# Kernel optimization log

Hardware: AMD Instinct MI355X
Metric: run time of the kernel (lower is better)

The kernel has to match this reference:

```python
import jax, jax.numpy as jnp
import numpy as np

N_NODES = 50000


def setup_inputs() -> dict:
    key = jax.random.key(0)
    k1, k2, k3, k4 = jax.random.split(key, 4)
    x = jax.random.normal(k1, (N_NODES, 256), dtype=jnp.float32)
    edge_index = jax.random.randint(k2, (2, 800000), 0, N_NODES, dtype=jnp.int64)
    W1 = jax.random.normal(k3, (256, 128), dtype=jnp.float32) * (1.0 / np.sqrt(256))
    b1 = jnp.zeros((128,), dtype=jnp.float32)
    W2 = jax.random.normal(k4, (128, 16), dtype=jnp.float32) * (1.0 / np.sqrt(128))
    b2 = jnp.zeros((16,), dtype=jnp.float32)
    return {"x": x, "edge_index": edge_index, "W1": W1, "b1": b1, "W2": W2, "b2": b2}


def _gcn_norm(edge_index, num_nodes):
    # add self-loops, then symmetric normalization D^-1/2 A D^-1/2 (PyG GCNConv default)
    loop = jnp.arange(num_nodes, dtype=edge_index.dtype)
    src = jnp.concatenate([edge_index[0], loop])
    dst = jnp.concatenate([edge_index[1], loop])
    deg = jax.ops.segment_sum(jnp.ones_like(dst, dtype=jnp.float32), dst, num_segments=num_nodes)
    dinv = jnp.where(deg > 0, jax.lax.rsqrt(deg), 0.0)
    norm = dinv[src] * dinv[dst]  # [E+N]
    return src, dst, norm


def _gcn_conv(h, W, b, src, dst, norm, num_nodes):
    h = h @ W                             # linear before propagate
    msg = h[src] * norm[:, None]          # gather + edge scaling
    agg = jax.ops.segment_sum(msg, dst, num_segments=num_nodes)  # scatter-add
    return agg + b


def reference(x, edge_index, W1, b1, W2, b2):
    n = x.shape[0]
    src, dst, norm = _gcn_norm(edge_index, n)
    h = jax.nn.relu(_gcn_conv(x, W1, b1, src, dst, norm, n))
    # F.dropout(training=False) is identity in eval mode
    out = _gcn_conv(h, W2, b2, src, dst, norm, n)
    return jax.nn.log_softmax(out, axis=1)
```

## Files before the change

### kernel.cpp

```cpp
#include <hip/hip_runtime.h>
#include <hip/hip_bf16.h>
#include <math.h>


#define FIN 256
#define FH  128
#define FO  16
#define ECH_LOG 13
#define ECH (1 << ECH_LOG)
#define NCHUNK 98
#define WPH 6272

typedef unsigned int uint;
typedef unsigned short ushort;
typedef __attribute__((ext_vector_type(8))) short bf16x8;
typedef __attribute__((ext_vector_type(4))) float f32x4;

static __device__ __forceinline__ ushort f2bf(float f) {
    __hip_bfloat16 b = __float2bfloat16(f);
    return *reinterpret_cast<ushort*>(&b);
}
static __device__ __forceinline__ float bf2f(ushort u) {
    return __uint_as_float(((uint)u) << 16);
}

__global__ __launch_bounds__(256) void GCN_wprep_k(const float* __restrict__ W1,
                                                   ushort* __restrict__ whT,
                                                   ushort* __restrict__ wlT) {
    int i = blockIdx.x * 256 + threadIdx.x;
    int k = i >> 7, c = i & 127;
    float w = W1[i];
    ushort hh = f2bf(w);
    ushort hl = f2bf(w - bf2f(hh));
    whT[c * 256 + k] = hh;
    wlT[c * 256 + k] = hl;
}

#define G1_BR 64
#define G1_KC 32

__global__ __launch_bounds__(256, 4) void GCN_histgemm_k(
        const float* __restrict__ x, const ushort* __restrict__ whT,
        const ushort* __restrict__ wlT, ushort* __restrict__ h1,
        const int* __restrict__ edge, uint* __restrict__ cw,
        int* __restrict__ rank,
        int N, int E, int nHist, int nWords, int wph) {
    __shared__ __align__(16) char smem[WPH * 4];
    int tid = threadIdx.x;

    if ((int)blockIdx.x < nHist) {
        int bid = blockIdx.x;
        int half = bid & 1;
        int c = bid >> 1;
        uint* lh = (uint*)smem;
        int w0 = half * wph;
        int wlim = nWords - w0; if (wlim > wph) wlim = wph;
        for (int j = tid; j < wlim; j += 256) lh[j] = 0;
        __syncthreads();
        int base = c << ECH_LOG;
        int lim = base + ECH; if (lim > E) lim = E;
        for (int i = base + tid; i < lim; i += 256) {
            int d = edge[E + i];
            int wd = (d >> 2) - w0;
            if ((unsigned)wd < (unsigned)wlim) {
                int sh = (d & 3) << 3;
                uint old = atomicAdd(&lh[wd], 1u << sh);
                rank[i] = (int)((old >> sh) & 0xFFu);
            }
        }
        __syncthreads();
        for (int j = tid; j < wlim; j += 256)
            cw[(size_t)c * nWords + w0 + j] = lh[j];
        return;
    }

    ushort* xh_s = (ushort*)smem;
    ushort* wh_s = (ushort*)(smem + 4096);
    ushort* wl_s = (ushort*)(smem + 12288);
    int row0 = (blockIdx.x - nHist) * G1_BR;
    int ln = tid & 63;
    int w  = tid >> 6;
    int ln15 = ln & 15;
    int q16  = ln >> 4;

    f32x4 acc[4][2];
    #pragma unroll
    for (int mr = 0; mr < 4; mr++)
        #pragma unroll
        for (int nc = 0; nc < 2; nc++) acc[mr][nc] = (f32x4){0.f, 0.f, 0.f, 0.f};

    for (int kc = 0; kc < FIN; kc += G1_KC) {
        #pragma unroll
        for (int j = 0; j < 2; j++) {
            int u = tid + j * 256;
            int r = u >> 3, kq = u & 7;
            int gr = row0 + r;
            float4 v = make_float4(0.f, 0.f, 0.f, 0.f);
            if (gr < N) v = *(const float4*)&x[(size_t)gr * FIN + kc + kq * 4];
            uint2 hw;
            hw.x = (uint)f2bf(v.x) | ((uint)f2bf(v.y) << 16);
            hw.y = (uint)f2bf(v.z) | ((uint)f2bf(v.w) << 16);
            int byte = (r * 64 + kq * 8) ^ (((r >> 1) & 3) << 4);
            *(uint2*)((char*)xh_s + byte) = hw;
        }
        #pragma unroll
        for (int j = 0; j < 2; j++) {
            int u = tid + j * 256;
            int c = u >> 2, ku = u & 3;
            uint4 vh = *(const uint4*)&whT[(size_t)c * 256 + kc + ku * 8];
            uint4 vl = *(const uint4*)&wlT[(size_t)c * 256 + kc + ku * 8];
            int byte = (c * 64 + ku * 16) ^ (((c >> 1) & 3) << 4);
            *(uint4*)((char*)wh_s + byte) = vh;
            *(uint4*)((char*)wl_s + byte) = vl;
        }
        __syncthreads();

        bf16x8 ah[4], bh[2], bl[2];
        #pragma unroll
        for (int mr = 0; mr < 4; mr++) {
            int r = mr * 16 + ln15;
            int byte = r * 64 + ((q16 * 16) ^ (((r >> 1) & 3) << 4));
            ah[mr] = *(const bf16x8*)((const char*)xh_s + byte);
        }
        #pragma unroll
        for (int nc = 0; nc < 2; nc++) {
            int c = w * 32 + nc * 16 + ln15;
            int byte = c * 64 + ((q16 * 16) ^ (((c >> 1) & 3) << 4));
            bh[nc] = *(const bf16x8*)((const char*)wh_s + byte);
            bl[nc] = *(const bf16x8*)((const char*)wl_s + byte);
        }
        #pragma unroll
        for (int mr = 0; mr < 4; mr++)
            #pragma unroll
            for (int nc = 0; nc < 2; nc++) {
                acc[mr][nc] = __builtin_amdgcn_mfma_f32_16x16x32_bf16(
                    ah[mr], bh[nc], acc[mr][nc], 0, 0, 0);
                acc[mr][nc] = __builtin_amdgcn_mfma_f32_16x16x32_bf16(
                    ah[mr], bl[nc], acc[mr][nc], 0, 0, 0);
            }
        __syncthreads();
    }

    #pragma unroll
    for (int mr = 0; mr < 4; mr++) {
        #pragma unroll
        for (int nc = 0; nc < 2; nc++) {
            int cw2 = w * 32 + nc * 16 + ln15;
            #pragma unroll
            for (int j = 0; j < 4; j++) {
                int gr = row0 + mr * 16 + q16 * 4 + j;
                if (gr < N) h1[(size_t)gr * FH + cw2] = f2bf(acc[mr][nc][j]);
            }
        }
    }
}

__global__ __launch_bounds__(256) void GCN_chpfx_k(uint* __restrict__ cw,
                                                   int* __restrict__ count,
                                                   int* __restrict__ bsum,
                                                   int N, int nWords) {
    __shared__ int part[4][64][4];
    __shared__ int red[64];
    int tid = threadIdx.x;
    int wl = tid & 63, g = tid >> 6;
    int w = blockIdx.x * 64 + wl;
    int c0 = g * 25;
    int c1 = c0 + 25; if (c1 > NCHUNK) c1 = NCHUNK;

    int s0 = 0, s1 = 0, s2 = 0, s3 = 0;
    if (w < nWords) {
        for (int c = c0; c < c1; c++) {
            uint v = cw[(size_t)c * nWords + w];
            s0 += (int)(v & 0xFFu);
            s1 += (int)((v >> 8) & 0xFFu);
            s2 += (int)((v >> 16) & 0xFFu);
            s3 += (int)((v >> 24) & 0xFFu);
        }
    }
    part[g][wl][0] = s0; part[g][wl][1] = s1;
    part[g][wl][2] = s2; part[g][wl][3] = s3;
    __syncthreads();

    int b0 = 0, b1 = 0, b2 = 0, b3 = 0;
    for (int gg = 0; gg < g; gg++) {
        b0 += part[gg][wl][0]; b1 += part[gg][wl][1];
        b2 += part[gg][wl][2]; b3 += part[gg][wl][3];
    }
    if (w < nWords) {
        uint r0 = (uint)b0, r1 = (uint)b1, r2 = (uint)b2, r3 = (uint)b3;
        for (int c = c0; c < c1; c++) {
            uint* p = &cw[(size_t)c * nWords + w];
            uint v = *p;
            *p = (r0 & 0xFFu) | ((r1 & 0xFFu) << 8) | ((r2 & 0xFFu) << 16) | ((r3 & 0xFFu) << 24);
            r0 += v & 0xFFu;
            r1 += (v >> 8) & 0xFFu;
            r2 += (v >> 16) & 0xFFu;
            r3 += (v >> 24) & 0xFFu;
        }
    }
    int local = 0;
    if (g == 3 && w < nWords) {
        int t0 = b0 + s0, t1 = b1 + s1, t2 = b2 + s2, t3 = b3 + s3;
        int d0 = 4 * w;
        if (d0 + 0 < N) count[d0 + 0] = t0;
        if (d0 + 1 < N) count[d0 + 1] = t1;
        if (d0 + 2 < N) count[d0 + 2] = t2;
        if (d0 + 3 < N) count[d0 + 3] = t3;
        local = t0 + t1 + t2 + t3 + 4;
    }
    if (g == 3) red[wl] = local;
    __syncthreads();
    if (tid < 32) { red[tid] += red[tid + 32]; }
    __syncthreads();
    if (tid < 16) { red[tid] += red[tid + 16]; }
    __syncthreads();
    if (tid < 8) { red[tid] += red[tid + 8]; }
    __syncthreads();
    if (tid < 4) { red[tid] += red[tid + 4]; }
    __syncthreads();
    if (tid == 0) bsum[blockIdx.x] = red[0] + red[1] + red[2] + red[3];
}

__global__ __launch_bounds__(256) void GCN_scan2_k(const int* __restrict__ count,
                                                   const int* __restrict__ bsum,
                                                   int2* __restrict__ rd2,
                                                   int2* __restrict__ edata, int N) {
    int tid = threadIdx.x;
    int b = blockIdx.x;
    int d = b * 256 + tid;
    int cnt1 = (d < N) ? count[d] + 1 : 0;

    __shared__ int red[256];
    int offp = 0;
    for (int t = tid; t < b; t += 256) offp += bsum[t];
    red[tid] = offp;
    __syncthreads();
    for (int st = 128; st > 0; st >>= 1) {
        if (tid < st) red[tid] += red[tid + st];
        __syncthreads();
    }
    int blockOff = red[0];
    __syncthreads();

    __shared__ int ssum[256];
    ssum[tid] = cnt1;
    __syncthreads();
    for (int off = 1; off < 256; off <<= 1) {
        int t = (tid >= off) ? ssum[tid - off] : 0;
        __syncthreads();
        ssum[tid] += t;
        __syncthreads();
    }
    int r = blockOff + ssum[tid] - cnt1;

    if (d < N) {
        float dv = rsqrtf((float)cnt1);
        rd2[d] = make_int2(r, __float_as_int(dv));
        edata[r] = make_int2(d, __float_as_int(dv * dv));
    }
    if (b == gridDim.x - 1 && tid == 255) rd2[N] = make_int2(blockOff + ssum[255], 0);
}

__global__ __launch_bounds__(256) void GCN_fill_k(const int* __restrict__ edge,
                                                  const int* __restrict__ rank,
                                                  const uint* __restrict__ cw,
                                                  const int2* __restrict__ rd2,
                                                  int2* __restrict__ edata,
                                                  int E, int nWords) {
    int i = blockIdx.x * 256 + threadIdx.x;
    if (i >= E) return;
    int s = edge[i];
    int d = edge[E + i];
    int rk = rank[i];
    int c = i >> ECH_LOG;
    uint pw = cw[(size_t)c * nWords + (d >> 2)];
    int pfx = (int)((pw >> ((d & 3) << 3)) & 0xFFu);
    int2 rdd = rd2[d];
    float ds = __int_as_float(rd2[s].y);
    edata[rdd.x + 1 + pfx + rk] =
        make_int2(s, __float_as_int(ds * __int_as_float(rdd.y)));
}

__global__ __launch_bounds__(256) void GCN_agg1gemm2_k(
        const ushort* __restrict__ h1, const int2* __restrict__ rd2,
        const int2* __restrict__ ed, const float* __restrict__ b1,
        const float* __restrict__ W2, ushort* __restrict__ h2b, int N) {
    __shared__ float w2s[FH][FO];
    __shared__ float hs[16][FH + 4];
    int tid = threadIdx.x;
    #pragma unroll
    for (int j = 0; j < (FH * FO) / 256; j++) {
        int i = tid + j * 256;
        w2s[i >> 4][i & 15] = W2[i];
    }

    int node0 = blockIdx.x * 16;
    int local = tid >> 4;
    int j = tid & 15;
    int node = node0 + local;

    if (node < N) {
        int beg = rd2[node].x, end = rd2[node + 1].x;
        const uint4* hp = (const uint4*)h1;

        float a[8];
        #pragma unroll
        for (int t = 0; t < 8; t++) a[t] = 0.f;

        int i = beg;
        for (; i + 8 <= end; i += 8) {
            int2 e[8];
            uint4 gg[8];
            #pragma unroll
            for (int t = 0; t < 8; t++) e[t] = ed[i + t];
            #pragma unroll
            for (int t = 0; t < 8; t++) gg[t] = hp[(size_t)e[t].x * 16 + j];
            #pragma unroll
            for (int t = 0; t < 8; t++) {
                float w = __int_as_float(e[t].y);
                #pragma unroll
                for (int q = 0; q < 4; q++) {
                    uint u = (&gg[t].x)[q];
                    a[q*2+0] += __uint_as_float(u << 16) * w;
                    a[q*2+1] += __uint_as_float(u & 0xFFFF0000u) * w;
                }
            }
        }
        for (; i + 4 <= end; i += 4) {
            int2 e0 = ed[i + 0], e1 = ed[i + 1], e2 = ed[i + 2], e3 = ed[i + 3];
            float w0 = __int_as_float(e0.y), w1 = __int_as_float(e1.y);
            float w2 = __int_as_float(e2.y), w3 = __int_as_float(e3.y);
            uint4 g0 = hp[(size_t)e0.x * 16 + j];
            uint4 g1 = hp[(size_t)e1.x * 16 + j];
            uint4 g2 = hp[(size_t)e2.x * 16 + j];
            uint4 g3 = hp[(size_t)e3.x * 16 + j];
            #pragma unroll
            for (int q = 0; q < 4; q++) {
                uint u0 = (&g0.x)[q], u1 = (&g1.x)[q], u2 = (&g2.x)[q], u3 = (&g3.x)[q];
                a[q*2+0] += __uint_as_float(u0 << 16) * w0;
                a[q*2+1] += __uint_as_float(u0 & 0xFFFF0000u) * w0;
                a[q*2+0] += __uint_as_float(u1 << 16) * w1;
                a[q*2+1] += __uint_as_float(u1 & 0xFFFF0000u) * w1;
                a[q*2+0] += __uint_as_float(u2 << 16) * w2;
                a[q*2+1] += __uint_as_float(u2 & 0xFFFF0000u) * w2;
                a[q*2+0] += __uint_as_float(u3 << 16) * w3;
                a[q*2+1] += __uint_as_float(u3 & 0xFFFF0000u) * w3;
            }
        }
        for (; i < end; i++) {
            int2 e = ed[i];
            float w = __int_as_float(e.y);
            uint4 g = hp[(size_t)e.x * 16 + j];
            #pragma unroll
            for (int q = 0; q < 4; q++) {
                uint u = (&g.x)[q];
                a[q*2+0] += __uint_as_float(u << 16) * w;
                a[q*2+1] += __uint_as_float(u & 0xFFFF0000u) * w;
            }
        }

        const float4* bp = (const float4*)b1;
        float4 bb0 = bp[j * 2 + 0];
        float4 bb1 = bp[j * 2 + 1];
        float4 o0, o1;
        o0.x = fmaxf(a[0] + bb0.x, 0.f);
        o0.y = fmaxf(a[1] + bb0.y, 0.f);
        o0.z = fmaxf(a[2] + bb0.z, 0.f);
        o0.w = fmaxf(a[3] + bb0.w, 0.f);
        o1.x = fmaxf(a[4] + bb1.x, 0.f);
        o1.y = fmaxf(a[5] + bb1.y, 0.f);
        o1.z = fmaxf(a[6] + bb1.z, 0.f);
        o1.w = fmaxf(a[7] + bb1.w, 0.f);
        *(float4*)&hs[local][j * 8 + 0] = o0;
        *(float4*)&hs[local][j * 8 + 4] = o1;
    }
    __syncthreads();

    float acc = 0.f;
    #pragma unroll 8
    for (int k = 0; k < FH; k++) acc += hs[local][k] * w2s[k][j];
    if (node < N) h2b[(size_t)node * FO + j] = f2bf(acc);
}

__global__ __launch_bounds__(256) void GCN_agg2_k(const ushort* __restrict__ h2b,
                                                  const int2* __restrict__ rd2,
                                                  const int2* __restrict__ ed,
                                                  const float* __restrict__ b2,
                                                  float* __restrict__ out, int N) {
    int tid = threadIdx.x;
    int node = blockIdx.x * 32 + (tid >> 3);
    if (node >= N) return;
    int f2 = tid & 7;
    int beg = rd2[node].x, end = rd2[node + 1].x;
    const uint* hp = (const uint*)h2b;
    float a0 = 0.f, a1 = 0.f;
    int i = beg;
    for (; i + 8 <= end; i += 8) {
        int2 e[8];
        uint u[8];
        #pragma unroll
        for (int t = 0; t < 8; t++) e[t] = ed[i + t];
        #pragma unroll
        for (int t = 0; t < 8; t++) u[t] = hp[(size_t)e[t].x * 8 + f2];
        #pragma unroll
        for (int t = 0; t < 8; t++) {
            float w = __int_as_float(e[t].y);
            a0 += __uint_as_float(u[t] << 16) * w;
            a1 += __uint_as_float(u[t] & 0xFFFF0000u) * w;
        }
    }
    for (; i + 4 <= end; i += 4) {
        int2 e0 = ed[i + 0], e1 = ed[i + 1], e2 = ed[i + 2], e3 = ed[i + 3];
        uint u0 = hp[(size_t)e0.x * 8 + f2];
        uint u1 = hp[(size_t)e1.x * 8 + f2];
        uint u2 = hp[(size_t)e2.x * 8 + f2];
        uint u3 = hp[(size_t)e3.x * 8 + f2];
        float w0 = __int_as_float(e0.y), w1 = __int_as_float(e1.y);
        float w2 = __int_as_float(e2.y), w3 = __int_as_float(e3.y);
        a0 += __uint_as_float(u0 << 16) * w0 + __uint_as_float(u1 << 16) * w1
            + __uint_as_float(u2 << 16) * w2 + __uint_as_float(u3 << 16) * w3;
        a1 += __uint_as_float(u0 & 0xFFFF0000u) * w0 + __uint_as_float(u1 & 0xFFFF0000u) * w1
            + __uint_as_float(u2 & 0xFFFF0000u) * w2 + __uint_as_float(u3 & 0xFFFF0000u) * w3;
    }
    for (; i < end; i++) {
        int2 e = ed[i];
        uint u = hp[(size_t)e.x * 8 + f2];
        float w = __int_as_float(e.y);
        a0 += __uint_as_float(u << 16) * w;
        a1 += __uint_as_float(u & 0xFFFF0000u) * w;
    }
    float2 bb = ((const float2*)b2)[f2];
    float v0 = a0 + bb.x;
    float v1 = a1 + bb.y;
    float mx = fmaxf(v0, v1);
    #pragma unroll
    for (int m = 4; m >= 1; m >>= 1) mx = fmaxf(mx, __shfl_xor(mx, m, 8));
    float s = expf(v0 - mx) + expf(v1 - mx);
    #pragma unroll
    for (int m = 4; m >= 1; m >>= 1) s += __shfl_xor(s, m, 8);
    float ls = logf(s);
    float2 o = make_float2(v0 - mx - ls, v1 - mx - ls);
    ((float2*)out)[(size_t)node * 8 + f2] = o;
}

extern "C" void kernel_launch(void* const* d_in, const int* in_sizes, int n_in,
                              void* d_out, int out_size, void* d_ws, size_t ws_size,
                              hipStream_t stream) {
    (void)n_in; (void)out_size; (void)ws_size;
    const float* x  = (const float*)d_in[0];
    const int*   edp = (const int*)d_in[1];
    const float* W1 = (const float*)d_in[2];
    const float* b1 = (const float*)d_in[3];
    const float* W2 = (const float*)d_in[4];
    const float* b2 = (const float*)d_in[5];
    float* out = (float*)d_out;

    int N = in_sizes[0] / FIN;
    int E = in_sizes[1] / 2;
    int M = E + N;
    int nWords = (N + 3) / 4;
    int wph = (nWords + 1) / 2;
    int nScanBlocks = (N + 255) / 256;
    int nChpfx = (nWords + 63) / 64;

    char* p = (char*)d_ws;
    auto take = [&](size_t bytes) -> char* {
        char* r = p;
        p += (bytes + 255) & ~(size_t)255;
        return r;
    };
    int*    count  = (int*)take((size_t)N * 4);
    int*    rank   = (int*)take((size_t)E * 4);
    uint*   cw     = (uint*)take((size_t)NCHUNK * nWords * 4);
    int2*   rd2    = (int2*)take((size_t)(N + 1) * 8);
    int*    bsum   = (int*)take((size_t)nChpfx * 4);
    int2*   edata  = (int2*)take((size_t)M * 8);
    ushort* whT    = (ushort*)take((size_t)FH * FIN * 2);
    ushort* wlT    = (ushort*)take((size_t)FH * FIN * 2);
    ushort* h1     = (ushort*)take((size_t)N * FH * 2);
    ushort* h2b    = (ushort*)take((size_t)N * FO * 2);

    int eBlocks = (E + 255) / 256;
    int nGemm   = (N + G1_BR - 1) / G1_BR;
    int nHist   = 2 * NCHUNK;

    GCN_wprep_k<<<(FIN * FH) / 256, 256, 0, stream>>>(W1, whT, wlT);
    GCN_histgemm_k<<<nHist + nGemm, 256, 0, stream>>>(
        x, whT, wlT, h1, edp, cw, rank, N, E, nHist, nWords, wph);
    GCN_chpfx_k<<<nChpfx, 256, 0, stream>>>(cw, count, bsum, N, nWords);
    GCN_scan2_k<<<nScanBlocks, 256, 0, stream>>>(count, bsum, rd2, edata, N);
    GCN_fill_k<<<eBlocks, 256, 0, stream>>>(edp, rank, cw, rd2, edata, E, nWords);
    GCN_agg1gemm2_k<<<(N + 15) / 16, 256, 0, stream>>>(h1, rd2, edata, b1, W2, h2b, N);
    GCN_agg2_k<<<(N + 31) / 32, 256, 0, stream>>>(h2b, rd2, edata, b2, out, N);
}
```

Before: 113.4 us.

## Regroup kernels: fuse histogram with weight prep, fill with GEMM, pack edge data

Histogram blocks are merged with W1 bf16 split preparation into one launch, and the CSR fill is merged with the first GEMM. The GEMM therefore no longer shares a launch with the histogram's large shared-memory footprint, which should improve its occupancy. Edge records are packed into 32 bits, a 16-bit source index plus a bf16 normalisation weight, and per-edge ranks shrink to bytes, cutting memory traffic in fill and both aggregations. The trade-offs are lower precision on the edge weights and a source index capped at 65535, which holds for the test's 50000 nodes but not in general.

```diff
diff --git a/kernel.cpp b/kernel.cpp
--- a/kernel.cpp
+++ b/kernel.cpp
@@ -13,6 +13,7 @@
 
 typedef unsigned int uint;
 typedef unsigned short ushort;
+typedef unsigned char uchar;
 typedef __attribute__((ext_vector_type(8))) short bf16x8;
 typedef __attribute__((ext_vector_type(4))) float f32x4;
 
@@ -24,60 +25,189 @@
     return __uint_as_float(((uint)u) << 16);
 }
 
-__global__ __launch_bounds__(256) void GCN_wprep_k(const float* __restrict__ W1,
-                                                   ushort* __restrict__ whT,
-                                                   ushort* __restrict__ wlT) {
-    int i = blockIdx.x * 256 + threadIdx.x;
-    int k = i >> 7, c = i & 127;
-    float w = W1[i];
-    ushort hh = f2bf(w);
-    ushort hl = f2bf(w - bf2f(hh));
-    whT[c * 256 + k] = hh;
-    wlT[c * 256 + k] = hl;
+__global__ __launch_bounds__(256) void GCN_histwprep_k(
+        const int* __restrict__ edge, uint* __restrict__ cw,
+        uchar* __restrict__ rank8,
+        const float* __restrict__ W1, ushort* __restrict__ whT,
+        ushort* __restrict__ wlT,
+        int E, int nHist, int nWords, int wph) {
+    __shared__ uint lh[WPH];
+    int tid = threadIdx.x;
+
+    if ((int)blockIdx.x >= nHist) {
+        int i = (blockIdx.x - nHist) * 256 + tid;
+        int k = i >> 7, c = i & 127;
+        float w = W1[i];
+        ushort hh = f2bf(w);
+        ushort hl = f2bf(w - bf2f(hh));
+        whT[c * 256 + k] = hh;
+        wlT[c * 256 + k] = hl;
+        return;
+    }
+
+    int bid = blockIdx.x;
+    int half = bid & 1;
+    int c = bid >> 1;
+    int w0 = half * wph;
+    int wlim = nWords - w0; if (wlim > wph) wlim = wph;
+    for (int j = tid; j < wlim; j += 256) lh[j] = 0;
+    __syncthreads();
+    int base = c << ECH_LOG;
+    int lim = base + ECH; if (lim > E) lim = E;
+    for (int i = base + tid; i < lim; i += 256) {
+        int d = edge[E + i];
+        int wd = (d >> 2) - w0;
+        if ((unsigned)wd < (unsigned)wlim) {
+            int sh = (d & 3) << 3;
+            uint old = atomicAdd(&lh[wd], 1u << sh);
+            rank8[i] = (uchar)((old >> sh) & 0xFFu);
+        }
+    }
+    __syncthreads();
+    for (int j = tid; j < wlim; j += 256)
+        cw[(size_t)c * nWords + w0 + j] = lh[j];
+}
+
+__global__ __launch_bounds__(256) void GCN_chpfx_k(uint* __restrict__ cw,
+                                                   int* __restrict__ count,
+                                                   int* __restrict__ bsum,
+                                                   int N, int nWords) {
+    __shared__ int part[4][64][4];
+    __shared__ int red[64];
+    int tid = threadIdx.x;
+    int wl = tid & 63, g = tid >> 6;
+    int w = blockIdx.x * 64 + wl;
+    int c0 = g * 25;
+    int c1 = c0 + 25; if (c1 > NCHUNK) c1 = NCHUNK;
+
+    int s0 = 0, s1 = 0, s2 = 0, s3 = 0;
+    if (w < nWords) {
+        for (int c = c0; c < c1; c++) {
+            uint v = cw[(size_t)c * nWords + w];
+            s0 += (int)(v & 0xFFu);
+            s1 += (int)((v >> 8) & 0xFFu);
+            s2 += (int)((v >> 16) & 0xFFu);
+            s3 += (int)((v >> 24) & 0xFFu);
+        }
+    }
+    part[g][wl][0] = s0; part[g][wl][1] = s1;
+    part[g][wl][2] = s2; part[g][wl][3] = s3;
+    __syncthreads();
+
+    int b0 = 0, b1 = 0, b2 = 0, b3 = 0;
+    for (int gg = 0; gg < g; gg++) {
+        b0 += part[gg][wl][0]; b1 += part[gg][wl][1];
+        b2 += part[gg][wl][2]; b3 += part[gg][wl][3];
+    }
+    if (w < nWords) {
+        uint r0 = (uint)b0, r1 = (uint)b1, r2 = (uint)b2, r3 = (uint)b3;
+        for (int c = c0; c < c1; c++) {
+            uint* p = &cw[(size_t)c * nWords + w];
+            uint v = *p;
+            *p = (r0 & 0xFFu) | ((r1 & 0xFFu) << 8) | ((r2 & 0xFFu) << 16) | ((r3 & 0xFFu) << 24);
+            r0 += v & 0xFFu;
+            r1 += (v >> 8) & 0xFFu;
+            r2 += (v >> 16) & 0xFFu;
+            r3 += (v >> 24) & 0xFFu;
+        }
+    }
+    int local = 0;
+    if (g == 3 && w < nWords) {
+        int t0 = b0 + s0, t1 = b1 + s1, t2 = b2 + s2, t3 = b3 + s3;
+        int d0 = 4 * w;
+        if (d0 + 0 < N) count[d0 + 0] = t0;
+        if (d0 + 1 < N) count[d0 + 1] = t1;
+        if (d0 + 2 < N) count[d0 + 2] = t2;
+        if (d0 + 3 < N) count[d0 + 3] = t3;
+        local = t0 + t1 + t2 + t3 + 4;
+    }
+    if (g == 3) red[wl] = local;
+    __syncthreads();
+    if (tid < 32) { red[tid] += red[tid + 32]; }
+    __syncthreads();
+    if (tid < 16) { red[tid] += red[tid + 16]; }
+    __syncthreads();
+    if (tid < 8) { red[tid] += red[tid + 8]; }
+    __syncthreads();
+    if (tid < 4) { red[tid] += red[tid + 4]; }
+    __syncthreads();
+    if (tid == 0) bsum[blockIdx.x] = red[0] + red[1] + red[2] + red[3];
+}
+
+__global__ __launch_bounds__(256) void GCN_scan2_k(const int* __restrict__ count,
+                                                   const int* __restrict__ bsum,
+                                                   int2* __restrict__ rd2,
+                                                   uint* __restrict__ edata, int N) {
+    int tid = threadIdx.x;
+    int b = blockIdx.x;
+    int d = b * 256 + tid;
+    int cnt1 = (d < N) ? count[d] + 1 : 0;
+
+    __shared__ int red[256];
+    int offp = 0;
+    for (int t = tid; t < b; t += 256) offp += bsum[t];
+    red[tid] = offp;
+    __syncthreads();
+    for (int st = 128; st > 0; st >>= 1) {
+        if (tid < st) red[tid] += red[tid + st];
+        __syncthreads();
+    }
+    int blockOff = red[0];
+    __syncthreads();
+
+    __shared__ int ssum[256];
+    ssum[tid] = cnt1;
+    __syncthreads();
+    for (int off = 1; off < 256; off <<= 1) {
+        int t = (tid >= off) ? ssum[tid - off] : 0;
+        __syncthreads();
+        ssum[tid] += t;
+        __syncthreads();
+    }
+    int r = blockOff + ssum[tid] - cnt1;
+
+    if (d < N) {
+        float dv = rsqrtf((float)cnt1);
+        rd2[d] = make_int2(r, __float_as_int(dv));
+        edata[r] = (uint)d | ((uint)f2bf(dv * dv) << 16);
+    }
+    if (b == gridDim.x - 1 && tid == 255) rd2[N] = make_int2(blockOff + ssum[255], 0);
 }
 
 #define G1_BR 64
 #define G1_KC 32
 
-__global__ __launch_bounds__(256, 4) void GCN_histgemm_k(
+__global__ __launch_bounds__(256, 4) void GCN_fillgemm_k(
+        const int* __restrict__ edge, const uchar* __restrict__ rank8,
+        const uint* __restrict__ cw, const int2* __restrict__ rd2,
+        uint* __restrict__ edata,
         const float* __restrict__ x, const ushort* __restrict__ whT,
         const ushort* __restrict__ wlT, ushort* __restrict__ h1,
-        const int* __restrict__ edge, uint* __restrict__ cw,
-        int* __restrict__ rank,
-        int N, int E, int nHist, int nWords, int wph) {
-    __shared__ __align__(16) char smem[WPH * 4];
-    int tid = threadIdx.x;
-
-    if ((int)blockIdx.x < nHist) {
-        int bid = blockIdx.x;
-        int half = bid & 1;
-        int c = bid >> 1;
-        uint* lh = (uint*)smem;
-        int w0 = half * wph;
-        int wlim = nWords - w0; if (wlim > wph) wlim = wph;
-        for (int j = tid; j < wlim; j += 256) lh[j] = 0;
-        __syncthreads();
-        int base = c << ECH_LOG;
-        int lim = base + ECH; if (lim > E) lim = E;
-        for (int i = base + tid; i < lim; i += 256) {
+        int N, int E, int nFill, int nWords) {
+    __shared__ __align__(16) char smem[20480];
+    int tid = threadIdx.x;
+
+    if ((int)blockIdx.x < nFill) {
+        int i = blockIdx.x * 256 + tid;
+        if (i < E) {
+            int s = edge[i];
             int d = edge[E + i];
-            int wd = (d >> 2) - w0;
-            if ((unsigned)wd < (unsigned)wlim) {
-                int sh = (d & 3) << 3;
-                uint old = atomicAdd(&lh[wd], 1u << sh);
-                rank[i] = (int)((old >> sh) & 0xFFu);
-            }
-        }
-        __syncthreads();
-        for (int j = tid; j < wlim; j += 256)
-            cw[(size_t)c * nWords + w0 + j] = lh[j];
+            int rk = (int)rank8[i];
+            int c = i >> ECH_LOG;
+            uint pw = cw[(size_t)c * nWords + (d >> 2)];
+            int pfx = (int)((pw >> ((d & 3) << 3)) & 0xFFu);
+            int2 rdd = rd2[d];
+            float ds = __int_as_float(rd2[s].y);
+            float nr = ds * __int_as_float(rdd.y);
+            edata[rdd.x + 1 + pfx + rk] = (uint)s | ((uint)f2bf(nr) << 16);
+        }
         return;
     }
 
     ushort* xh_s = (ushort*)smem;
     ushort* wh_s = (ushort*)(smem + 4096);
     ushort* wl_s = (ushort*)(smem + 12288);
-    int row0 = (blockIdx.x - nHist) * G1_BR;
+    int row0 = (blockIdx.x - nFill) * G1_BR;
     int ln = tid & 63;
     int w  = tid >> 6;
     int ln15 = ln & 15;
@@ -155,135 +285,9 @@
     }
 }
 
-__global__ __launch_bounds__(256) void GCN_chpfx_k(uint* __restrict__ cw,
-                                                   int* __restrict__ count,
-                                                   int* __restrict__ bsum,
-                                                   int N, int nWords) {
-    __shared__ int part[4][64][4];
-    __shared__ int red[64];
-    int tid = threadIdx.x;
-    int wl = tid & 63, g = tid >> 6;
-    int w = blockIdx.x * 64 + wl;
-    int c0 = g * 25;
-    int c1 = c0 + 25; if (c1 > NCHUNK) c1 = NCHUNK;
-
-    int s0 = 0, s1 = 0, s2 = 0, s3 = 0;
-    if (w < nWords) {
-        for (int c = c0; c < c1; c++) {
-            uint v = cw[(size_t)c * nWords + w];
-            s0 += (int)(v & 0xFFu);
-            s1 += (int)((v >> 8) & 0xFFu);
-            s2 += (int)((v >> 16) & 0xFFu);
-            s3 += (int)((v >> 24) & 0xFFu);
-        }
-    }
-    part[g][wl][0] = s0; part[g][wl][1] = s1;
-    part[g][wl][2] = s2; part[g][wl][3] = s3;
-    __syncthreads();
-
-    int b0 = 0, b1 = 0, b2 = 0, b3 = 0;
-    for (int gg = 0; gg < g; gg++) {
-        b0 += part[gg][wl][0]; b1 += part[gg][wl][1];
-        b2 += part[gg][wl][2]; b3 += part[gg][wl][3];
-    }
-    if (w < nWords) {
-        uint r0 = (uint)b0, r1 = (uint)b1, r2 = (uint)b2, r3 = (uint)b3;
-        for (int c = c0; c < c1; c++) {
-            uint* p = &cw[(size_t)c * nWords + w];
-            uint v = *p;
-            *p = (r0 & 0xFFu) | ((r1 & 0xFFu) << 8) | ((r2 & 0xFFu) << 16) | ((r3 & 0xFFu) << 24);
-            r0 += v & 0xFFu;
-            r1 += (v >> 8) & 0xFFu;
-            r2 += (v >> 16) & 0xFFu;
-            r3 += (v >> 24) & 0xFFu;
-        }
-    }
-    int local = 0;
-    if (g == 3 && w < nWords) {
-        int t0 = b0 + s0, t1 = b1 + s1, t2 = b2 + s2, t3 = b3 + s3;
-        int d0 = 4 * w;
-        if (d0 + 0 < N) count[d0 + 0] = t0;
-        if (d0 + 1 < N) count[d0 + 1] = t1;
-        if (d0 + 2 < N) count[d0 + 2] = t2;
-        if (d0 + 3 < N) count[d0 + 3] = t3;
-        local = t0 + t1 + t2 + t3 + 4;
-    }
-    if (g == 3) red[wl] = local;
-    __syncthreads();
-    if (tid < 32) { red[tid] += red[tid + 32]; }
-    __syncthreads();
-    if (tid < 16) { red[tid] += red[tid + 16]; }
-    __syncthreads();
-    if (tid < 8) { red[tid] += red[tid + 8]; }
-    __syncthreads();
-    if (tid < 4) { red[tid] += red[tid + 4]; }
-    __syncthreads();
-    if (tid == 0) bsum[blockIdx.x] = red[0] + red[1] + red[2] + red[3];
-}
-
-__global__ __launch_bounds__(256) void GCN_scan2_k(const int* __restrict__ count,
-                                                   const int* __restrict__ bsum,
-                                                   int2* __restrict__ rd2,
-                                                   int2* __restrict__ edata, int N) {
-    int tid = threadIdx.x;
-    int b = blockIdx.x;
-    int d = b * 256 + tid;
-    int cnt1 = (d < N) ? count[d] + 1 : 0;
-
-    __shared__ int red[256];
-    int offp = 0;
-    for (int t = tid; t < b; t += 256) offp += bsum[t];
-    red[tid] = offp;
-    __syncthreads();
-    for (int st = 128; st > 0; st >>= 1) {
-        if (tid < st) red[tid] += red[tid + st];
-        __syncthreads();
-    }
-    int blockOff = red[0];
-    __syncthreads();
-
-    __shared__ int ssum[256];
-    ssum[tid] = cnt1;
-    __syncthreads();
-    for (int off = 1; off < 256; off <<= 1) {
-        int t = (tid >= off) ? ssum[tid - off] : 0;
-        __syncthreads();
-        ssum[tid] += t;
-        __syncthreads();
-    }
-    int r = blockOff + ssum[tid] - cnt1;
-
-    if (d < N) {
-        float dv = rsqrtf((float)cnt1);
-        rd2[d] = make_int2(r, __float_as_int(dv));
-        edata[r] = make_int2(d, __float_as_int(dv * dv));
-    }
-    if (b == gridDim.x - 1 && tid == 255) rd2[N] = make_int2(blockOff + ssum[255], 0);
-}
-
-__global__ __launch_bounds__(256) void GCN_fill_k(const int* __restrict__ edge,
-                                                  const int* __restrict__ rank,
-                                                  const uint* __restrict__ cw,
-                                                  const int2* __restrict__ rd2,
-                                                  int2* __restrict__ edata,
-                                                  int E, int nWords) {
-    int i = blockIdx.x * 256 + threadIdx.x;
-    if (i >= E) return;
-    int s = edge[i];
-    int d = edge[E + i];
-    int rk = rank[i];
-    int c = i >> ECH_LOG;
-    uint pw = cw[(size_t)c * nWords + (d >> 2)];
-    int pfx = (int)((pw >> ((d & 3) << 3)) & 0xFFu);
-    int2 rdd = rd2[d];
-    float ds = __int_as_float(rd2[s].y);
-    edata[rdd.x + 1 + pfx + rk] =
-        make_int2(s, __float_as_int(ds * __int_as_float(rdd.y)));
-}
-
 __global__ __launch_bounds__(256) void GCN_agg1gemm2_k(
         const ushort* __restrict__ h1, const int2* __restrict__ rd2,
-        const int2* __restrict__ ed, const float* __restrict__ b1,
+        const uint* __restrict__ ed, const float* __restrict__ b1,
         const float* __restrict__ W2, ushort* __restrict__ h2b, int N) {
     __shared__ float w2s[FH][FO];
     __shared__ float hs[16][FH + 4];
@@ -309,15 +313,15 @@
 
         int i = beg;
         for (; i + 8 <= end; i += 8) {
-            int2 e[8];
+            uint e[8];
             uint4 gg[8];
             #pragma unroll
             for (int t = 0; t < 8; t++) e[t] = ed[i + t];
             #pragma unroll
-            for (int t = 0; t < 8; t++) gg[t] = hp[(size_t)e[t].x * 16 + j];
+            for (int t = 0; t < 8; t++) gg[t] = hp[(size_t)(e[t] & 0xFFFFu) * 16 + j];
             #pragma unroll
             for (int t = 0; t < 8; t++) {
-                float w = __int_as_float(e[t].y);
+                float w = bf2f((ushort)(e[t] >> 16));
                 #pragma unroll
                 for (int q = 0; q < 4; q++) {
                     uint u = (&gg[t].x)[q];
@@ -326,31 +330,10 @@
                 }
             }
         }
-        for (; i + 4 <= end; i += 4) {
-            int2 e0 = ed[i + 0], e1 = ed[i + 1], e2 = ed[i + 2], e3 = ed[i + 3];
-            float w0 = __int_as_float(e0.y), w1 = __int_as_float(e1.y);
-            float w2 = __int_as_float(e2.y), w3 = __int_as_float(e3.y);
-            uint4 g0 = hp[(size_t)e0.x * 16 + j];
-            uint4 g1 = hp[(size_t)e1.x * 16 + j];
-            uint4 g2 = hp[(size_t)e2.x * 16 + j];
-            uint4 g3 = hp[(size_t)e3.x * 16 + j];
-            #pragma unroll
-            for (int q = 0; q < 4; q++) {
-                uint u0 = (&g0.x)[q], u1 = (&g1.x)[q], u2 = (&g2.x)[q], u3 = (&g3.x)[q];
-                a[q*2+0] += __uint_as_float(u0 << 16) * w0;
-                a[q*2+1] += __uint_as_float(u0 & 0xFFFF0000u) * w0;
-                a[q*2+0] += __uint_as_float(u1 << 16) * w1;
-                a[q*2+1] += __uint_as_float(u1 & 0xFFFF0000u) * w1;
-                a[q*2+0] += __uint_as_float(u2 << 16) * w2;
-                a[q*2+1] += __uint_as_float(u2 & 0xFFFF0000u) * w2;
-                a[q*2+0] += __uint_as_float(u3 << 16) * w3;
-                a[q*2+1] += __uint_as_float(u3 & 0xFFFF0000u) * w3;
-            }
-        }
         for (; i < end; i++) {
-            int2 e = ed[i];
-            float w = __int_as_float(e.y);
-            uint4 g = hp[(size_t)e.x * 16 + j];
+            uint e = ed[i];
+            float w = bf2f((ushort)(e >> 16));
+            uint4 g = hp[(size_t)(e & 0xFFFFu) * 16 + j];
             #pragma unroll
             for (int q = 0; q < 4; q++) {
                 uint u = (&g.x)[q];
@@ -384,7 +367,7 @@
 
 __global__ __launch_bounds__(256) void GCN_agg2_k(const ushort* __restrict__ h2b,
                                                   const int2* __restrict__ rd2,
-                                                  const int2* __restrict__ ed,
+                                                  const uint* __restrict__ ed,
                                                   const float* __restrict__ b2,
                                                   float* __restrict__ out, int N) {
     int tid = threadIdx.x;
@@ -396,36 +379,23 @@
     float a0 = 0.f, a1 = 0.f;
     int i = beg;
     for (; i + 8 <= end; i += 8) {
-        int2 e[8];
+        uint e[8];
         uint u[8];
         #pragma unroll
         for (int t = 0; t < 8; t++) e[t] = ed[i + t];
         #pragma unroll
-        for (int t = 0; t < 8; t++) u[t] = hp[(size_t)e[t].x * 8 + f2];
+        for (int t = 0; t < 8; t++) u[t] = hp[(size_t)(e[t] & 0xFFFFu) * 8 + f2];
         #pragma unroll
         for (int t = 0; t < 8; t++) {
-            float w = __int_as_float(e[t].y);
+            float w = bf2f((ushort)(e[t] >> 16));
             a0 += __uint_as_float(u[t] << 16) * w;
             a1 += __uint_as_float(u[t] & 0xFFFF0000u) * w;
         }
     }
-    for (; i + 4 <= end; i += 4) {
-        int2 e0 = ed[i + 0], e1 = ed[i + 1], e2 = ed[i + 2], e3 = ed[i + 3];
-        uint u0 = hp[(size_t)e0.x * 8 + f2];
-        uint u1 = hp[(size_t)e1.x * 8 + f2];
-        uint u2 = hp[(size_t)e2.x * 8 + f2];
-        uint u3 = hp[(size_t)e3.x * 8 + f2];
-        float w0 = __int_as_float(e0.y), w1 = __int_as_float(e1.y);
-        float w2 = __int_as_float(e2.y), w3 = __int_as_float(e3.y);
-        a0 += __uint_as_float(u0 << 16) * w0 + __uint_as_float(u1 << 16) * w1
-            + __uint_as_float(u2 << 16) * w2 + __uint_as_float(u3 << 16) * w3;
-        a1 += __uint_as_float(u0 & 0xFFFF0000u) * w0 + __uint_as_float(u1 & 0xFFFF0000u) * w1
-            + __uint_as_float(u2 & 0xFFFF0000u) * w2 + __uint_as_float(u3 & 0xFFFF0000u) * w3;
-    }
     for (; i < end; i++) {
-        int2 e = ed[i];
-        uint u = hp[(size_t)e.x * 8 + f2];
-        float w = __int_as_float(e.y);
+        uint e = ed[i];
+        uint u = hp[(size_t)(e & 0xFFFFu) * 8 + f2];
+        float w = bf2f((ushort)(e >> 16));
         a0 += __uint_as_float(u << 16) * w;
         a1 += __uint_as_float(u & 0xFFFF0000u) * w;
     }
@@ -470,11 +440,11 @@
         return r;
     };
     int*    count  = (int*)take((size_t)N * 4);
-    int*    rank   = (int*)take((size_t)E * 4);
+    uchar*  rank8  = (uchar*)take((size_t)E);
     uint*   cw     = (uint*)take((size_t)NCHUNK * nWords * 4);
     int2*   rd2    = (int2*)take((size_t)(N + 1) * 8);
     int*    bsum   = (int*)take((size_t)nChpfx * 4);
-    int2*   edata  = (int2*)take((size_t)M * 8);
+    uint*   edata  = (uint*)take((size_t)M * 4);
     ushort* whT    = (ushort*)take((size_t)FH * FIN * 2);
     ushort* wlT    = (ushort*)take((size_t)FH * FIN * 2);
     ushort* h1     = (ushort*)take((size_t)N * FH * 2);
@@ -484,12 +454,12 @@
     int nGemm   = (N + G1_BR - 1) / G1_BR;
     int nHist   = 2 * NCHUNK;
 
-    GCN_wprep_k<<<(FIN * FH) / 256, 256, 0, stream>>>(W1, whT, wlT);
-    GCN_histgemm_k<<<nHist + nGemm, 256, 0, stream>>>(
-        x, whT, wlT, h1, edp, cw, rank, N, E, nHist, nWords, wph);
+    GCN_histwprep_k<<<nHist + (FIN * FH) / 256, 256, 0, stream>>>(
+        edp, cw, rank8, W1, whT, wlT, E, nHist, nWords, wph);
     GCN_chpfx_k<<<nChpfx, 256, 0, stream>>>(cw, count, bsum, N, nWords);
     GCN_scan2_k<<<nScanBlocks, 256, 0, stream>>>(count, bsum, rd2, edata, N);
-    GCN_fill_k<<<eBlocks, 256, 0, stream>>>(edp, rank, cw, rd2, edata, E, nWords);
+    GCN_fillgemm_k<<<eBlocks + nGemm, 256, 0, stream>>>(
+        edp, rank8, cw, rd2, edata, x, whT, wlT, h1, N, E, eBlocks, nWords);
     GCN_agg1gemm2_k<<<(N + 15) / 16, 256, 0, stream>>>(h1, rd2, edata, b1, W2, h2b, N);
     GCN_agg2_k<<<(N + 31) / 32, 256, 0, stream>>>(h2b, rd2, edata, b2, out, N);
 }
```

New measurement: 119.1 us. 1.05x slower.
